# Kernel tuning notes

Measured on AMD Instinct MI355X. Metric: run time of the kernel, lower is better.

The kernel has to match this reference:

```python
import jax, jax.numpy as jnp
import numpy as np

N_HEAD = 16
SCALE = True
NEG = 10000.0


def setup_inputs() -> dict:
    key = jax.random.key(0)
    ks = jax.random.split(key, 5)
    B, S, D = 4, 1024, 1024
    x = jax.random.normal(ks[0], (B, S, D), dtype=jnp.float32)
    # GPT-2 Conv1D weights: W has shape [in, out], init ~N(0, 0.02)
    w_attn = jax.random.normal(ks[1], (D, 3 * D), dtype=jnp.float32) * 0.02
    b_attn = jnp.zeros((3 * D,), dtype=jnp.float32)
    w_proj = jax.random.normal(ks[2], (D, D), dtype=jnp.float32) * 0.02
    b_proj = jnp.zeros((D,), dtype=jnp.float32)
    return {"x": x, "w_attn": w_attn, "b_attn": b_attn,
            "w_proj": w_proj, "b_proj": b_proj}


def reference(x, w_attn, b_attn, w_proj, b_proj):
    B, S, D = x.shape
    H = N_HEAD
    hd = D // H
    # c_attn: Conv1D == x @ W + b
    qkv = jnp.einsum('bsd,de->bse', x, w_attn) + b_attn
    q, k, v = jnp.split(qkv, 3, axis=-1)
    # split heads -> [B, H, S, hd]
    q = q.reshape(B, S, H, hd).transpose(0, 2, 1, 3)
    k = k.reshape(B, S, H, hd).transpose(0, 2, 1, 3)
    v = v.reshape(B, S, H, hd).transpose(0, 2, 1, 3)
    # scores [B, H, S, S]
    w = jnp.einsum('bhqd,bhkd->bhqk', q, k)
    if SCALE:
        w = w / jnp.sqrt(jnp.float32(hd))
    # multiplicative causal mask: w*b - 10000*(1-b)
    bmask = jnp.tril(jnp.ones((S, S), dtype=w.dtype))[None, None]
    w = w * bmask - NEG * (1.0 - bmask)
    w = jax.nn.softmax(w, axis=-1)
    # attn_pdrop = 0 -> dropout is identity
    a = jnp.einsum('bhqk,bhkd->bhqd', w, v)
    # merge heads
    a = a.transpose(0, 2, 1, 3).reshape(B, S, D)
    # c_proj; resid_pdrop = 0
    out = jnp.einsum('bsd,de->bse', a, w_proj) + b_proj
    return out
```

## Files before the change

kernel.cpp:

```cpp
#include <hip/hip_runtime.h>
#include <hip/hip_bf16.h>


typedef __bf16 bf16x8 __attribute__((ext_vector_type(8)));
typedef __bf16 bf16x4 __attribute__((ext_vector_type(4)));
typedef float f32x4 __attribute__((ext_vector_type(4)));

__device__ __forceinline__ void load_lds16(const void* g, void* l) {
  __builtin_amdgcn_global_load_lds(
      (const __attribute__((address_space(1))) void*)g,
      (__attribute__((address_space(3))) void*)l, 16, 0, 0);
}

#define BAR8 asm volatile("s_barrier" ::: "memory")
#define LGKM0 asm volatile("s_waitcnt lgkmcnt(0)" ::: "memory")

__global__ __launch_bounds__(256) void prep(
    const float* __restrict__ x, const float* __restrict__ w_attn,
    const float* __restrict__ w_proj, __bf16* __restrict__ Xb,
    __bf16* __restrict__ WT_attn, __bf16* __restrict__ WT_proj) {
  __shared__ __bf16 tile[32][33];
  const int blk = blockIdx.x;
  const int tid = threadIdx.x;
  if (blk < 4096) {
    const float* W;
    __bf16* WT;
    int n0, k0, N;
    if (blk < 3072) {
      W = w_attn; WT = WT_attn; N = 3072;
      n0 = (blk % 96) * 32; k0 = (blk / 96) * 32;
    } else {
      W = w_proj; WT = WT_proj; N = 1024;
      const int t = blk - 3072;
      n0 = (t & 31) * 32; k0 = (t >> 5) * 32;
    }
    const int tx = tid & 31, ty = tid >> 5;
#pragma unroll
    for (int j = 0; j < 32; j += 8)
      tile[ty + j][tx] = (__bf16)W[(size_t)(k0 + ty + j) * N + n0 + tx];
    __syncthreads();
#pragma unroll
    for (int j = 0; j < 32; j += 8)
      WT[(size_t)(n0 + ty + j) * 1024 + k0 + tx] = tile[tx][ty + j];
  } else {
    const size_t i = (size_t)(blk - 4096) * 4096 + tid * 16;
    const float4* xp = (const float4*)(x + i);
    float4 a = xp[0], b = xp[1], c = xp[2], d = xp[3];
    bf16x8 o0, o1;
    o0[0] = (__bf16)a.x; o0[1] = (__bf16)a.y; o0[2] = (__bf16)a.z; o0[3] = (__bf16)a.w;
    o0[4] = (__bf16)b.x; o0[5] = (__bf16)b.y; o0[6] = (__bf16)b.z; o0[7] = (__bf16)b.w;
    o1[0] = (__bf16)c.x; o1[1] = (__bf16)c.y; o1[2] = (__bf16)c.z; o1[3] = (__bf16)c.w;
    o1[4] = (__bf16)d.x; o1[5] = (__bf16)d.y; o1[6] = (__bf16)d.z; o1[7] = (__bf16)d.w;
    *(bf16x8*)(Xb + i) = o0;
    *(bf16x8*)(Xb + i + 8) = o1;
  }
}


#define STG(GMAT, GROW0, K0, LOFF)                                             \
  _Pragma("unroll") for (int i_ = 0; i_ < 2; ++i_)                             \
    load_lds16((GMAT) + (size_t)((GROW0) + i_ * 64 + wave * 8 + srow) * 1024 + \
                   (K0) + schunk * 8,                                          \
               smem8 + (LOFF) + (i_ * 64 + wave * 8) * 64);

#define LDA8(BASE, MH)                                                         \
  _Pragma("unroll") for (int m_ = 0; m_ < 4; ++m_)                             \
  _Pragma("unroll") for (int kk_ = 0; kk_ < 2; ++kk_)                          \
    af[m_][kk_] = *(const bf16x8*)((BASE) + ((MH)*64 + m_ * 16 + l16) * 64 +   \
                                   (((kk_ * 4 + quad) ^ rsw) * 8));

#define LDB8(BASE, NLO)                                                        \
  _Pragma("unroll") for (int n_ = 0; n_ < 2; ++n_)                             \
  _Pragma("unroll") for (int kk_ = 0; kk_ < 2; ++kk_)                          \
    bf[(NLO) + n_][kk_] =                                                      \
        *(const bf16x8*)((BASE) + ((waveN & 1) * 64 + ((NLO) + n_) * 16 +      \
                                   l16) * 64 +                                 \
                         (((kk_ * 4 + quad) ^ rsw) * 8));

#define MFMA_HALF(MH, NLO)                                                     \
  __builtin_amdgcn_s_setprio(1);                                               \
  _Pragma("unroll") for (int m_ = 0; m_ < 4; ++m_)                             \
  _Pragma("unroll") for (int n_ = 0; n_ < 2; ++n_) {                           \
    acc[(MH)*4 + m_][(NLO) + n_] = __builtin_amdgcn_mfma_f32_16x16x32_bf16(    \
        af[m_][0], bf[(NLO) + n_][0], acc[(MH)*4 + m_][(NLO) + n_], 0, 0, 0);  \
    acc[(MH)*4 + m_][(NLO) + n_] = __builtin_amdgcn_mfma_f32_16x16x32_bf16(    \
        af[m_][1], bf[(NLO) + n_][1], acc[(MH)*4 + m_][(NLO) + n_], 0, 0, 0);  \
  }                                                                            \
  __builtin_amdgcn_s_setprio(0);

__global__ __launch_bounds__(512, 2) void gemm_qkv8(
    const __bf16* __restrict__ A, const __bf16* __restrict__ BT,
    const float* __restrict__ bias, __bf16* __restrict__ Qp,
    __bf16* __restrict__ Kp, __bf16* __restrict__ Vt) {
  __shared__ __bf16 smem8[65536];
  const int tid = threadIdx.x;
  const int lane = tid & 63;
  const int wave = tid >> 6;
  const int waveM = wave >> 2;
  const int waveN = wave & 3;
  const int l16 = lane & 15;
  const int quad = lane >> 4;
  const int rsw = l16 & 7;
  const int srow = lane >> 3;
  const int schunk = (lane & 7) ^ srow;

  const int bid = blockIdx.x;
  const int c = bid & 7, l = bid >> 3;
  const int tm = (c >> 1) * 4 + l / 6;
  const int tn = (c & 1) * 6 + l % 6;
  const int rowBase = tm * 256;
  const int colBase = tn * 256;

  const __bf16* aRd = smem8 + waveM * 8192;
  const __bf16* bRd = smem8 + 16384 + (waveN >> 1) * 8192;

  f32x4 acc[8][4] = {};
  bf16x8 af[4][2], bf[4][2];

  STG(A, rowBase, 0, 0);
  STG(A, rowBase + 128, 0, 8192);
  STG(BT, colBase, 0, 16384);
  STG(BT, colBase + 128, 0, 24576);
  STG(BT, colBase, 64, 32768 + 16384);
  STG(BT, colBase + 128, 64, 32768 + 24576);
  STG(A, rowBase, 64, 32768);
  asm volatile("s_waitcnt vmcnt(6)" ::: "memory");
  BAR8;

  for (int t = 0; t < 8; ++t) {
    const int kO = t * 128 + 64;
    const int kS2 = t * 128 + 128;
    const int kS3 = t * 128 + 192;
    const bool s2 = kS2 < 1024;
    const bool s3 = kS3 < 1024;

    LDA8(aRd, 0);
    LDB8(bRd, 0);
    STG(A, rowBase + 128, kO, 32768 + 8192);
    BAR8; LGKM0;
    MFMA_HALF(0, 0);
    BAR8;

    LDB8(bRd, 2);
    BAR8; LGKM0;
    MFMA_HALF(0, 2);
    BAR8;

    LDA8(aRd, 1);
    if (s2) { STG(BT, colBase, kS2, 16384); }
    BAR8; LGKM0;
    MFMA_HALF(1, 2);
    BAR8;

    if (s2) {
      STG(BT, colBase + 128, kS2, 24576);
      STG(A, rowBase, kS2, 0);
      asm volatile("s_waitcnt vmcnt(6)" ::: "memory");
    } else {
      asm volatile("s_waitcnt vmcnt(0)" ::: "memory");
    }
    BAR8;
    MFMA_HALF(1, 0);
    BAR8;

    LDA8(aRd + 32768, 0);
    LDB8(bRd + 32768, 0);
    if (s2) { STG(A, rowBase + 128, kS2, 8192); }
    BAR8; LGKM0;
    MFMA_HALF(0, 0);
    BAR8;

    LDB8(bRd + 32768, 2);
    BAR8; LGKM0;
    MFMA_HALF(0, 2);
    BAR8;

    LDA8(aRd + 32768, 1);
    if (s3) { STG(BT, colBase, kS3, 32768 + 16384); }
    BAR8; LGKM0;
    MFMA_HALF(1, 2);
    BAR8;

    if (s3) {
      STG(BT, colBase + 128, kS3, 32768 + 24576);
      STG(A, rowBase, kS3, 32768);
    }
    asm volatile("s_waitcnt vmcnt(6)" ::: "memory");
    BAR8;
    MFMA_HALF(1, 0);
    BAR8;
  }

  const int seg = colBase >> 10;
  if (seg == 2) {
#pragma unroll
    for (int mm = 0; mm < 8; ++mm) {
      const int r0 = waveM * 128 + mm * 16 + quad * 4;
#pragma unroll
      for (int n = 0; n < 4; ++n) {
        const int cR = waveN * 64 + n * 16 + l16;
        const float bv = bias[colBase + cR];
        bf16x4 pk;
#pragma unroll
        for (int r = 0; r < 4; ++r) pk[r] = (__bf16)(acc[mm][n][r] + bv);
        *(bf16x4*)(&smem8[cR * 256 + (r0 ^ (l16 << 4))]) = pk;
      }
    }
    __syncthreads();
    const int b_ = rowBase >> 10;
    const int s0 = rowBase & 1023;
    const int hBase = (colBase & 1023) >> 6;
    const int ch = lane & 31;
#pragma unroll
    for (int p = 0; p < 16; ++p) {
      const int c2 = p * 16 + wave * 2 + (lane >> 5);
      bf16x8 v =
          *(const bf16x8*)(&smem8[c2 * 256 + ((ch * 8) ^ ((c2 & 15) << 4))]);
      const int bhd = (b_ * 16 + hBase + (c2 >> 6)) * 64 + (c2 & 63);
      *(bf16x8*)(&Vt[(size_t)bhd * 1024 + s0 + ch * 8]) = v;
    }
  } else {
#pragma unroll
    for (int mm = 0; mm < 8; ++mm) {
      const int row0 = rowBase + waveM * 128 + mm * 16 + quad * 4;
#pragma unroll
      for (int n = 0; n < 4; ++n) {
        const int col = colBase + waveN * 64 + n * 16 + l16;
        const float bv = bias[col];
        const int cc = col & 1023;
        __bf16* dst = (seg == 0) ? Qp : Kp;
#pragma unroll
        for (int r = 0; r < 4; ++r) {
          const int row = row0 + r;
          const float v = acc[mm][n][r] + bv;
          const int bh = ((row >> 10) << 4) + (cc >> 6);
          dst[((size_t)bh << 16) + (size_t)(row & 1023) * 64 + (cc & 63)] =
              (__bf16)v;
        }
      }
    }
  }
}

__global__ __launch_bounds__(256) void gemm_out(
    const __bf16* __restrict__ A, const __bf16* __restrict__ BT,
    const float* __restrict__ bias, float* __restrict__ C) {
  __shared__ __bf16 sA[3][128 * 32];
  __shared__ __bf16 sB[3][128 * 32];
  const int tid = threadIdx.x;
  const int lane = tid & 63;
  const int wave = tid >> 6;
  const int waveM = wave >> 1, waveN = wave & 1;
  const int quad = lane >> 4;
  const int l16 = lane & 15;
  const int rowBase = blockIdx.x * 128;
  const int colBase = blockIdx.y * 128;
  const int rIn = lane >> 2;
  const int sIn = lane & 3;
  const int gc = sIn ^ (rIn & 3) ^ ((rIn >> 2) & 3);
  const int readSlot = quad ^ (l16 & 3) ^ ((l16 >> 2) & 3);
  f32x4 acc[4][4] = {};

#define GO_STAGE(bi, k0_)                                                      \
  _Pragma("unroll") for (int j_ = 0; j_ < 2; ++j_) {                           \
    const int rb = wave * 32 + j_ * 16;                                        \
    load_lds16(&A[(size_t)(rowBase + rb + rIn) * 1024 + (k0_) + gc * 8],       \
               &sA[bi][rb * 32]);                                              \
    load_lds16(&BT[(size_t)(colBase + rb + rIn) * 1024 + (k0_) + gc * 8],      \
               &sB[bi][rb * 32]);                                              \
  }

  GO_STAGE(0, 0);
  GO_STAGE(1, 32);
  asm volatile("s_waitcnt vmcnt(4)" ::: "memory");
  BAR8;

#pragma unroll
  for (int i = 0; i < 32; ++i) {
    if (i + 2 < 32) { GO_STAGE((i + 2) % 3, (i + 2) * 32); }
    const __bf16* sAc = sA[i % 3];
    const __bf16* sBc = sB[i % 3];
    bf16x8 af[4], bfr[4];
#pragma unroll
    for (int mt = 0; mt < 4; ++mt)
      af[mt] = *(const bf16x8*)(&sAc[(waveM * 64 + mt * 16 + l16) * 32 +
                                     readSlot * 8]);
#pragma unroll
    for (int nt = 0; nt < 4; ++nt)
      bfr[nt] = *(const bf16x8*)(&sBc[(waveN * 64 + nt * 16 + l16) * 32 +
                                      readSlot * 8]);
    __builtin_amdgcn_s_setprio(1);
#pragma unroll
    for (int mt = 0; mt < 4; ++mt)
#pragma unroll
      for (int nt = 0; nt < 4; ++nt)
        acc[mt][nt] = __builtin_amdgcn_mfma_f32_16x16x32_bf16(
            af[mt], bfr[nt], acc[mt][nt], 0, 0, 0);
    __builtin_amdgcn_s_setprio(0);
    if (i + 1 < 32) {
      if (i + 2 < 32) {
        asm volatile("s_waitcnt vmcnt(4)" ::: "memory");
      } else {
        asm volatile("s_waitcnt vmcnt(0)" ::: "memory");
      }
      BAR8;
    }
  }

#pragma unroll
  for (int mt = 0; mt < 4; ++mt) {
    const int row = rowBase + waveM * 64 + mt * 16 + quad * 4;
#pragma unroll
    for (int nt = 0; nt < 4; ++nt) {
      const int col = colBase + waveN * 64 + nt * 16 + l16;
      const float bv = bias[col];
#pragma unroll
      for (int r = 0; r < 4; ++r)
        C[(size_t)(row + r) * 1024 + col] = acc[mt][nt][r] + bv;
    }
  }
}

__global__ __launch_bounds__(256, 4) void attn_mfma(
    const __bf16* __restrict__ Qp, const __bf16* __restrict__ Kp,
    const __bf16* __restrict__ VT, __bf16* __restrict__ Aout) {
  __shared__ __bf16 sK[128 * 64];
  __shared__ __bf16 sV[64 * 128];
  __shared__ __bf16 sP[4 * 16 * 64];

  const int tid = threadIdx.x;
  const int lane = tid & 63;
  const int wave = tid >> 6;
  const int quad = lane >> 4;
  const int l16 = lane & 15;
  const int swq = l16 & 7;

  const int bh = blockIdx.x & 63;
  const int qt = 15 - (blockIdx.x >> 6);
  const int b = bh >> 4, h = bh & 15;
  const int qb = qt * 64;
  const int ktmax = qt >> 1;

  const __bf16* Qb = Qp + ((size_t)bh << 16);
  const __bf16* Kb = Kp + ((size_t)bh << 16);
  const __bf16* VTb = VT + (size_t)bh * 64 * 1024;

  bf16x8 qA0, qA1;
  {
    const __bf16* qr = Qb + (size_t)(qb + wave * 16 + l16) * 64 + quad * 8;
    qA0 = *(const bf16x8*)qr;
    qA1 = *(const bf16x8*)(qr + 32);
  }

  f32x4 O[4] = {};
  float ps[4] = {0.f, 0.f, 0.f, 0.f};
  __bf16* pw = sP + wave * 1024;

  for (int kt = 0; kt <= ktmax; ++kt) {
    const int kb = kt * 128;
    __syncthreads();

#pragma unroll
    for (int i = 0; i < 4; ++i) {
      const int rb = wave * 32 + i * 8;
      load_lds16(Kb + (size_t)(kb + rb + (lane >> 3)) * 64 +
                     (((lane & 7) ^ ((lane >> 3) & 7)) << 3),
                 &sK[rb * 64]);
    }
#pragma unroll
    for (int i = 0; i < 4; ++i) {
      const int db = wave * 16 + i * 4;
      const int d = db + (lane >> 4);
      load_lds16(VTb + (size_t)d * 1024 + kb + (((lane & 15) ^ (d & 7)) << 3),
                 &sV[db * 128]);
    }
    __syncthreads();

    float sc[8][4];
    __builtin_amdgcn_s_setprio(1);
#pragma unroll
    for (int n = 0; n < 8; ++n) {
      const int key = n * 16 + l16;
      bf16x8 kB0 = *(const bf16x8*)(&sK[key * 64 + ((quad ^ swq) << 3)]);
      bf16x8 kB1 = *(const bf16x8*)(&sK[key * 64 + (((quad + 4) ^ swq) << 3)]);
      f32x4 cacc = {};
      cacc = __builtin_amdgcn_mfma_f32_16x16x32_bf16(qA0, kB0, cacc, 0, 0, 0);
      cacc = __builtin_amdgcn_mfma_f32_16x16x32_bf16(qA1, kB1, cacc, 0, 0, 0);
#pragma unroll
      for (int r = 0; r < 4; ++r) sc[n][r] = cacc[r] * 0.125f;
    }
    __builtin_amdgcn_s_setprio(0);

    if (kt == ktmax) {
#pragma unroll
      for (int n = 0; n < 8; ++n) {
        const int kg = kb + n * 16 + l16;
#pragma unroll
        for (int r = 0; r < 4; ++r)
          if (kg > qb + wave * 16 + quad * 4 + r) sc[n][r] = -1.0e30f;
      }
    }

#pragma unroll
    for (int n = 0; n < 8; ++n)
#pragma unroll
      for (int r = 0; r < 4; ++r) {
        float p = __expf(fminf(sc[n][r], 60.0f));
        sc[n][r] = p;
        ps[r] += p;
      }

    const int kb8 = l16 >> 3, lo = l16 & 7;
#pragma unroll
    for (int hf = 0; hf < 2; ++hf) {
#pragma unroll
      for (int n = 4 * hf; n < 4 * hf + 4; ++n) {
        const int crel = (n - 4 * hf) * 2 + kb8;
#pragma unroll
        for (int r = 0; r < 4; ++r) {
          const int q = quad * 4 + r;
          pw[q * 64 + ((crel ^ (q & 7)) << 3) + lo] = (__bf16)sc[n][r];
        }
      }
      __builtin_amdgcn_s_setprio(1);
#pragma unroll
      for (int cc = 2 * hf; cc < 2 * hf + 2; ++cc) {
        const int crel = (cc - 2 * hf) * 4 + quad;
        bf16x8 pA = *(const bf16x8*)(&pw[l16 * 64 + ((crel ^ swq) << 3)]);
#pragma unroll
        for (int nt = 0; nt < 4; ++nt) {
          bf16x8 vB = *(const bf16x8*)(&sV[(nt * 16 + l16) * 128 +
                                           (((cc * 4 + quad) ^ swq) << 3)]);
          O[nt] = __builtin_amdgcn_mfma_f32_16x16x32_bf16(pA, vB, O[nt], 0, 0, 0);
        }
      }
      __builtin_amdgcn_s_setprio(0);
    }
  }

  float inv[4];
#pragma unroll
  for (int r = 0; r < 4; ++r) {
    float pa = ps[r];
    pa += __shfl_xor(pa, 1);
    pa += __shfl_xor(pa, 2);
    pa += __shfl_xor(pa, 4);
    pa += __shfl_xor(pa, 8);
    inv[r] = 1.0f / pa;
  }
#pragma unroll
  for (int nt = 0; nt < 4; ++nt) {
#pragma unroll
    for (int r = 0; r < 4; ++r) {
      const int q = qb + wave * 16 + quad * 4 + r;
      Aout[((size_t)b * 1024 + q) * 1024 + h * 64 + nt * 16 + l16] =
          (__bf16)(O[nt][r] * inv[r]);
    }
  }
}

extern "C" void kernel_launch(void* const* d_in, const int* in_sizes, int n_in,
                              void* d_out, int out_size, void* d_ws,
                              size_t ws_size, hipStream_t stream) {
  const float* x      = (const float*)d_in[0];
  const float* w_attn = (const float*)d_in[1];
  const float* b_attn = (const float*)d_in[2];
  const float* w_proj = (const float*)d_in[3];
  const float* b_proj = (const float*)d_in[4];
  float* out = (float*)d_out;

  char* ws = (char*)d_ws;
  __bf16* WT_attn = (__bf16*)(ws);
  __bf16* WT_proj = (__bf16*)(ws + 6291456);
  __bf16* Xb      = (__bf16*)(ws + 8388608);
  __bf16* Qp      = (__bf16*)(ws + 16777216);
  __bf16* Kp      = (__bf16*)(ws + 25165824);
  __bf16* VT      = (__bf16*)(ws + 33554432);
  __bf16* Aattn   = (__bf16*)(ws + 41943040);

  prep<<<5120, 256, 0, stream>>>(x, w_attn, w_proj, Xb, WT_attn, WT_proj);
  gemm_qkv8<<<192, 512, 0, stream>>>(Xb, WT_attn, b_attn, Qp, Kp, VT);
  attn_mfma<<<1024, 256, 0, stream>>>(Qp, Kp, VT, Aattn);
  gemm_out<<<dim3(32, 8), 256, 0, stream>>>(Aattn, WT_proj, b_proj, out);
}
```

Baseline: 169.9 us.

## Pair causal query tiles per block and double-buffer K/V loads in attention

The attention kernel now runs 512 threads per block. Two groups of four waves each handle one of a pair of complementary query tiles (pr and 15-pr), which balances causal work and lets both tiles share the K/V tiles staged in LDS. K and V loads are double-buffered so the next tile is fetched while the current one is computed, and there is one barrier per iteration. The cost is twice the LDS per block and idle waves in the short-tile group once its causal range ends, since they still wait at every barrier.

```diff
diff --git a/kernel.cpp b/kernel.cpp
--- a/kernel.cpp
+++ b/kernel.cpp
@@ -321,25 +321,29 @@
   }
 }
 
-__global__ __launch_bounds__(256, 4) void attn_mfma(
+__global__ __launch_bounds__(512, 4) void attn_mfma(
     const __bf16* __restrict__ Qp, const __bf16* __restrict__ Kp,
     const __bf16* __restrict__ VT, __bf16* __restrict__ Aout) {
-  __shared__ __bf16 sK[128 * 64];
-  __shared__ __bf16 sV[64 * 128];
-  __shared__ __bf16 sP[4 * 16 * 64];
+  __shared__ __bf16 sK[2][128 * 64];
+  __shared__ __bf16 sV[2][64 * 128];
+  __shared__ __bf16 sP[8 * 16 * 64];
 
   const int tid = threadIdx.x;
   const int lane = tid & 63;
   const int wave = tid >> 6;
+  const int wq = wave & 3;
+  const int tileSel = wave >> 2;
   const int quad = lane >> 4;
   const int l16 = lane & 15;
   const int swq = l16 & 7;
 
   const int bh = blockIdx.x & 63;
-  const int qt = 15 - (blockIdx.x >> 6);
+  const int pr = blockIdx.x >> 6;
   const int b = bh >> 4, h = bh & 15;
-  const int qb = qt * 64;
-  const int ktmax = qt >> 1;
+  const int qbB = (15 - pr) * 64, qbA = pr * 64;
+  const int ktB_max = (15 - pr) >> 1, ktA_max = pr >> 1;
+  const int myQb = tileSel ? qbA : qbB;
+  const int myKt = tileSel ? ktA_max : ktB_max;
 
   const __bf16* Qb = Qp + ((size_t)bh << 16);
   const __bf16* Kb = Kp + ((size_t)bh << 16);
@@ -347,7 +351,7 @@
 
   bf16x8 qA0, qA1;
   {
-    const __bf16* qr = Qb + (size_t)(qb + wave * 16 + l16) * 64 + quad * 8;
+    const __bf16* qr = Qb + (size_t)(myQb + wq * 16 + l16) * 64 + quad * 8;
     qA0 = *(const bf16x8*)qr;
     qA1 = *(const bf16x8*)(qr + 32);
   }
@@ -356,85 +360,99 @@
   float ps[4] = {0.f, 0.f, 0.f, 0.f};
   __bf16* pw = sP + wave * 1024;
 
-  for (int kt = 0; kt <= ktmax; ++kt) {
+#define ATTN_STAGE(bi, kbase)                                                  \
+  _Pragma("unroll") for (int i_ = 0; i_ < 2; ++i_) {                           \
+    const int rb = wave * 16 + i_ * 8;                                         \
+    load_lds16(Kb + (size_t)((kbase) + rb + (lane >> 3)) * 64 +                \
+                   (((lane & 7) ^ ((lane >> 3) & 7)) << 3),                    \
+               &sK[bi][rb * 64]);                                              \
+  }                                                                            \
+  _Pragma("unroll") for (int i_ = 0; i_ < 2; ++i_) {                           \
+    const int db = wave * 8 + i_ * 4;                                          \
+    const int d = db + (lane >> 4);                                            \
+    load_lds16(VTb + (size_t)d * 1024 + (kbase) +                              \
+                   (((lane & 15) ^ (d & 7)) << 3),                             \
+               &sV[bi][db * 128]);                                             \
+  }
+
+  ATTN_STAGE(0, 0);
+  asm volatile("s_waitcnt vmcnt(0)" ::: "memory");
+  BAR8;
+
+  for (int kt = 0; kt <= ktB_max; ++kt) {
     const int kb = kt * 128;
-    __syncthreads();
-
-#pragma unroll
-    for (int i = 0; i < 4; ++i) {
-      const int rb = wave * 32 + i * 8;
-      load_lds16(Kb + (size_t)(kb + rb + (lane >> 3)) * 64 +
-                     (((lane & 7) ^ ((lane >> 3) & 7)) << 3),
-                 &sK[rb * 64]);
-    }
-#pragma unroll
-    for (int i = 0; i < 4; ++i) {
-      const int db = wave * 16 + i * 4;
-      const int d = db + (lane >> 4);
-      load_lds16(VTb + (size_t)d * 1024 + kb + (((lane & 15) ^ (d & 7)) << 3),
-                 &sV[db * 128]);
-    }
-    __syncthreads();
-
-    float sc[8][4];
-    __builtin_amdgcn_s_setprio(1);
-#pragma unroll
-    for (int n = 0; n < 8; ++n) {
-      const int key = n * 16 + l16;
-      bf16x8 kB0 = *(const bf16x8*)(&sK[key * 64 + ((quad ^ swq) << 3)]);
-      bf16x8 kB1 = *(const bf16x8*)(&sK[key * 64 + (((quad + 4) ^ swq) << 3)]);
-      f32x4 cacc = {};
-      cacc = __builtin_amdgcn_mfma_f32_16x16x32_bf16(qA0, kB0, cacc, 0, 0, 0);
-      cacc = __builtin_amdgcn_mfma_f32_16x16x32_bf16(qA1, kB1, cacc, 0, 0, 0);
-#pragma unroll
-      for (int r = 0; r < 4; ++r) sc[n][r] = cacc[r] * 0.125f;
-    }
-    __builtin_amdgcn_s_setprio(0);
-
-    if (kt == ktmax) {
+    const int cur = kt & 1;
+    if (kt < ktB_max) { ATTN_STAGE(cur ^ 1, kb + 128); }
+
+    if (kt <= myKt) {
+      const __bf16* skc = sK[cur];
+      const __bf16* svc = sV[cur];
+
+      float sc[8][4];
+      __builtin_amdgcn_s_setprio(1);
 #pragma unroll
       for (int n = 0; n < 8; ++n) {
-        const int kg = kb + n * 16 + l16;
-#pragma unroll
-        for (int r = 0; r < 4; ++r)
-          if (kg > qb + wave * 16 + quad * 4 + r) sc[n][r] = -1.0e30f;
+        const int key = n * 16 + l16;
+        bf16x8 kB0 = *(const bf16x8*)(&skc[key * 64 + ((quad ^ swq) << 3)]);
+        bf16x8 kB1 = *(const bf16x8*)(&skc[key * 64 + (((quad + 4) ^ swq) << 3)]);
+        f32x4 cacc = {};
+        cacc = __builtin_amdgcn_mfma_f32_16x16x32_bf16(qA0, kB0, cacc, 0, 0, 0);
+        cacc = __builtin_amdgcn_mfma_f32_16x16x32_bf16(qA1, kB1, cacc, 0, 0, 0);
+#pragma unroll
+        for (int r = 0; r < 4; ++r) sc[n][r] = cacc[r] * 0.125f;
       }
-    }
-
-#pragma unroll
-    for (int n = 0; n < 8; ++n)
-#pragma unroll
-      for (int r = 0; r < 4; ++r) {
-        float p = __expf(fminf(sc[n][r], 60.0f));
-        sc[n][r] = p;
-        ps[r] += p;
-      }
-
-    const int kb8 = l16 >> 3, lo = l16 & 7;
-#pragma unroll
-    for (int hf = 0; hf < 2; ++hf) {
-#pragma unroll
-      for (int n = 4 * hf; n < 4 * hf + 4; ++n) {
-        const int crel = (n - 4 * hf) * 2 + kb8;
-#pragma unroll
-        for (int r = 0; r < 4; ++r) {
-          const int q = quad * 4 + r;
-          pw[q * 64 + ((crel ^ (q & 7)) << 3) + lo] = (__bf16)sc[n][r];
+      __builtin_amdgcn_s_setprio(0);
+
+      if (kt == myKt) {
+#pragma unroll
+        for (int n = 0; n < 8; ++n) {
+          const int kg = kb + n * 16 + l16;
+#pragma unroll
+          for (int r = 0; r < 4; ++r)
+            if (kg > myQb + wq * 16 + quad * 4 + r) sc[n][r] = -1.0e30f;
         }
       }
-      __builtin_amdgcn_s_setprio(1);
-#pragma unroll
-      for (int cc = 2 * hf; cc < 2 * hf + 2; ++cc) {
-        const int crel = (cc - 2 * hf) * 4 + quad;
-        bf16x8 pA = *(const bf16x8*)(&pw[l16 * 64 + ((crel ^ swq) << 3)]);
-#pragma unroll
-        for (int nt = 0; nt < 4; ++nt) {
-          bf16x8 vB = *(const bf16x8*)(&sV[(nt * 16 + l16) * 128 +
-                                           (((cc * 4 + quad) ^ swq) << 3)]);
-          O[nt] = __builtin_amdgcn_mfma_f32_16x16x32_bf16(pA, vB, O[nt], 0, 0, 0);
+
+#pragma unroll
+      for (int n = 0; n < 8; ++n)
+#pragma unroll
+        for (int r = 0; r < 4; ++r) {
+          float p = __expf(fminf(sc[n][r], 60.0f));
+          sc[n][r] = p;
+          ps[r] += p;
         }
+
+      const int kb8 = l16 >> 3, lo = l16 & 7;
+#pragma unroll
+      for (int hf = 0; hf < 2; ++hf) {
+#pragma unroll
+        for (int n = 4 * hf; n < 4 * hf + 4; ++n) {
+          const int crel = (n - 4 * hf) * 2 + kb8;
+#pragma unroll
+          for (int r = 0; r < 4; ++r) {
+            const int q = quad * 4 + r;
+            pw[q * 64 + ((crel ^ (q & 7)) << 3) + lo] = (__bf16)sc[n][r];
+          }
+        }
+        __builtin_amdgcn_s_setprio(1);
+#pragma unroll
+        for (int cc = 2 * hf; cc < 2 * hf + 2; ++cc) {
+          const int crel = (cc - 2 * hf) * 4 + quad;
+          bf16x8 pA = *(const bf16x8*)(&pw[l16 * 64 + ((crel ^ swq) << 3)]);
+#pragma unroll
+          for (int nt = 0; nt < 4; ++nt) {
+            bf16x8 vB = *(const bf16x8*)(&svc[(nt * 16 + l16) * 128 +
+                                              (((cc * 4 + quad) ^ swq) << 3)]);
+            O[nt] = __builtin_amdgcn_mfma_f32_16x16x32_bf16(pA, vB, O[nt], 0, 0, 0);
+          }
+        }
+        __builtin_amdgcn_s_setprio(0);
       }
-      __builtin_amdgcn_s_setprio(0);
+    }
+
+    if (kt < ktB_max) {
+      asm volatile("s_waitcnt vmcnt(0)" ::: "memory");
+      BAR8;
     }
   }
 
@@ -452,7 +470,7 @@
   for (int nt = 0; nt < 4; ++nt) {
 #pragma unroll
     for (int r = 0; r < 4; ++r) {
-      const int q = qb + wave * 16 + quad * 4 + r;
+      const int q = myQb + wq * 16 + quad * 4 + r;
       Aout[((size_t)b * 1024 + q) * 1024 + h * 64 + nt * 16 + l16] =
           (__bf16)(O[nt][r] * inv[r]);
     }
@@ -480,6 +498,6 @@
 
   prep<<<5120, 256, 0, stream>>>(x, w_attn, w_proj, Xb, WT_attn, WT_proj);
   gemm_qkv8<<<192, 512, 0, stream>>>(Xb, WT_attn, b_attn, Qp, Kp, VT);
-  attn_mfma<<<1024, 256, 0, stream>>>(Qp, Kp, VT, Aattn);
+  attn_mfma<<<512, 512, 0, stream>>>(Qp, Kp, VT, Aattn);
   gemm_out<<<dim3(32, 8), 256, 0, stream>>>(Aattn, WT_proj, b_proj, out);
 }
```

Measured after the change: 163.5 us. -3.8%, faster.
